# Kernel optimization log

Measured on AMD Instinct MI355X. Metric: run time of the kernel, lower is better.

Reference implementation:

```python
import jax, jax.numpy as jnp
from jax import lax
import numpy as np

L = 2          # num_delimiter_layers
H = 8          # num q/kv heads
MIN_CL = 3
MAX_CL = 16

def rms_norm(x, w, eps=1e-6):
    return x * lax.rsqrt(jnp.mean(x * x, axis=-1, keepdims=True) + eps) * w

def rope(t):
    # t: [B, H, S, Dh], GPT-NeoX style half-split rotation, theta=10000
    Dh, S = t.shape[-1], t.shape[-2]
    half = Dh // 2
    inv = 1.0 / (10000.0 ** (jnp.arange(half, dtype=jnp.float32) / half))
    fr = jnp.arange(S, dtype=jnp.float32)[:, None] * inv  # [S, half]
    cos, sin = jnp.cos(fr), jnp.sin(fr)
    t1, t2 = t[..., :half], t[..., half:]
    return jnp.concatenate([t1 * cos - t2 * sin, t1 * sin + t2 * cos], axis=-1)

def chunk_ids_one(flags):
    # flags: [S] bool (probs > 0.5). Returns per-position chunk id and num chunks.
    S = flags.shape[0]
    # ends take value p+1 for flagged p; fallback to a single end at S-1 if none.
    has_end = jnp.zeros(S + 1, bool).at[1:].set(flags)
    fallback = jnp.zeros(S + 1, bool).at[S - 1].set(True)
    has_end = jnp.where(flags.any(), has_end, fallback)
    idx = jnp.where(has_end, jnp.arange(S + 1), S + 1)  # S+1 = sentinel > any cap
    nxt = lax.associative_scan(jnp.minimum, idx, reverse=True)  # nxt[e] = min end >= e
    def step(carry, t):
        cur_end, cid = carry
        def new(_):
            cap = jnp.minimum(t + MAX_CL, S)
            e = nxt[t + 1]                       # smallest end > t
            e = jnp.where(e <= cap, e, cap)
            e = jnp.where(e - t < MIN_CL, jnp.minimum(t + MIN_CL, S), e)
            return e, cid + 1
        new_end, new_cid = lax.cond(t == cur_end, new, lambda _: (cur_end, cid), None)
        return (new_end, new_cid), new_cid
    (_, last), ids = lax.scan(step, (jnp.int32(0), jnp.int32(-1)), jnp.arange(S, dtype=jnp.int32))
    return ids, last + 1

def _forward(x, ln1, Wq, Wk, Wv, Wo, ln2, W1, W2, head_w, head_b):
    B, S, D = x.shape
    Dh = D // H
    causal = jnp.tril(jnp.ones((S, S), bool))
    scale = 1.0 / np.sqrt(Dh)
    for l in range(L):
        h = rms_norm(x, ln1[l])
        def split_heads(t):
            return t.reshape(B, S, H, Dh).transpose(0, 2, 1, 3)
        q = rope(split_heads(h @ Wq[l]))
        k = rope(split_heads(h @ Wk[l]))
        v = split_heads(h @ Wv[l])
        scores = jnp.einsum('bhqd,bhkd->bhqk', q, k) * scale
        scores = jnp.where(causal, scores, jnp.finfo(scores.dtype).min)
        attn = jax.nn.softmax(scores, axis=-1)
        o = jnp.einsum('bhqk,bhkd->bhqd', attn, v)
        o = o.transpose(0, 2, 1, 3).reshape(B, S, D)
        x = x + o @ Wo[l]
        h = rms_norm(x, ln2[l])
        x = x + jax.nn.gelu(h @ W1[l], approximate=False) @ W2[l]
    logits = (x @ head_w).squeeze(-1) + head_b[0]
    probs = jax.nn.sigmoid(logits)
    chunk_len_loss = jnp.mean(jnp.sum(probs, axis=1))
    return x, probs, chunk_len_loss

def setup_inputs():
    key = jax.random.key(0)
    ks = jax.random.split(key, 10)
    B, S, D = 4, 2048, 512
    F = 4 * D
    sc = 0.02
    return {
        'x': jax.random.normal(ks[0], (B, S, D), jnp.float32),
        'x_ids': jax.random.randint(ks[1], (B, S), 0, 256),
        'ln1': jnp.ones((L, D), jnp.float32),
        'Wq': jax.random.normal(ks[2], (L, D, D), jnp.float32) * sc,
        'Wk': jax.random.normal(ks[3], (L, D, D), jnp.float32) * sc,
        'Wv': jax.random.normal(ks[4], (L, D, D), jnp.float32) * sc,
        'Wo': jax.random.normal(ks[5], (L, D, D), jnp.float32) * sc,
        'ln2': jnp.ones((L, D), jnp.float32),
        'W1': jax.random.normal(ks[6], (L, D, F), jnp.float32) * sc,
        'W2': jax.random.normal(ks[7], (L, F, D), jnp.float32) * sc,
        'head_w': jax.random.normal(ks[8], (D, 1), jnp.float32) * sc,
        'head_b': jnp.zeros((1,), jnp.float32),
    }

def reference(x, x_ids, ln1, Wq, Wk, Wv, Wo, ln2, W1, W2, head_w, head_b):
    B, S, D = x.shape
    x_t, probs, chunk_len_loss = _forward(x, ln1, Wq, Wk, Wv, Wo, ln2, W1, W2, head_w, head_b)
    flags = probs > 0.5
    ids, n_chunks = jax.vmap(chunk_ids_one)(flags)  # ids: [B,S] int32
    # chunks partition [0,S), so block-diagonal mask == chunk-id equality
    attention_masks = ids[:, :, None] == ids[:, None, :]
    # per-batch mean chunk length = S / num_chunks (lengths sum to S)
    avg_chunk_len = jnp.mean(jnp.float32(S) / n_chunks.astype(jnp.float32))
    return (x_t, x_ids, avg_chunk_len, attention_masks, chunk_len_loss)
```

## Files before the change

### kernel.cpp

```cpp
#include <hip/hip_runtime.h>
#include <math.h>

#define S_LEN 2048
#define DMODEL 512
#define NHEAD 8
#define DH 64
#define FDIM 2048

typedef unsigned short ushort_t;
typedef __attribute__((ext_vector_type(8))) short short8_t;
typedef __attribute__((ext_vector_type(4))) float float4_t;

#define MFMA16(a, b, c) __builtin_amdgcn_mfma_f32_16x16x32_bf16(a, b, c, 0, 0, 0)



__device__ __forceinline__ ushort_t f2bf(float x) {
    unsigned u = __float_as_uint(x);
    return (ushort_t)((u + 0x7fffu + ((u >> 16) & 1u)) >> 16);
}
__device__ __forceinline__ float bf2f(ushort_t h) {
    return __uint_as_float((unsigned)h << 16);
}
__device__ __forceinline__ float gelu_f(float x) {
    return 0.5f * x * (1.0f + erff(x * 0.70710678118654752440f));
}
__device__ __forceinline__ void gl_lds16(const void* g, void* l) {
    __builtin_amdgcn_global_load_lds(
        (const __attribute__((address_space(1))) void*)g,
        (__attribute__((address_space(3))) void*)l, 16, 0, 0);
}

template<int CTRL>
__device__ __forceinline__ float dpp_mov(float x) {
    return __int_as_float(__builtin_amdgcn_mov_dpp(__float_as_int(x), CTRL, 0xF, 0xF, true));
}
__device__ __forceinline__ float dpp_max16(float x) {
    x = fmaxf(x, dpp_mov<0xB1>(x));
    x = fmaxf(x, dpp_mov<0x4E>(x));
    x = fmaxf(x, dpp_mov<0x141>(x));
    x = fmaxf(x, dpp_mov<0x140>(x));
    return x;
}
__device__ __forceinline__ float dpp_sum16(float x) {
    x += dpp_mov<0xB1>(x);
    x += dpp_mov<0x4E>(x);
    x += dpp_mov<0x141>(x);
    x += dpp_mov<0x140>(x);
    return x;
}

__device__ __forceinline__ void stage_tile(const ushort_t* __restrict__ g, int rs,
                                           ushort_t* __restrict__ s, int w, int lane) {
    #pragma unroll
    for (int j = 0; j < 2; ++j) {
        const int c = (w * 2 + j) * 64 + lane;
        const int kk = c >> 8, row = (c >> 2) & 63, q = c & 3;
        const int qs = q ^ ((row >> 1) & 3);
        gl_lds16(g + (size_t)row * rs + kk * 32 + qs * 8, s + c * 8);
    }
}

__global__ __launch_bounds__(256) void copy_init_k(const int* __restrict__ x_ids,
                                                   float* __restrict__ out) {
    const int i = blockIdx.x * 256 + threadIdx.x;
    const int4 id4 = ((const int4*)x_ids)[i];
    ((float4*)out)[1048576 + i] =
        make_float4((float)id4.x, (float)id4.y, (float)id4.z, (float)id4.w);
    if (i == 0) { out[4202496] = 0.0f; out[20979713] = 0.0f; }
}

__global__ __launch_bounds__(256) void rope_tab_k(float2* __restrict__ tab) {
    const int i = blockIdx.x * 256 + threadIdx.x;
    const int s = i >> 5, f = i & 31;
    float inv = powf(10000.0f, -(float)f * (1.0f / 32.0f));
    float sn, cs;
    sincosf((float)s * inv, &sn, &cs);
    tab[i] = make_float2(cs, sn);
}

__global__ __launch_bounds__(256) void tsplit_all_k(const float* __restrict__ Wq,
                                                    const float* __restrict__ Wk,
                                                    const float* __restrict__ Wv,
                                                    const float* __restrict__ Wo,
                                                    const float* __restrict__ W1,
                                                    const float* __restrict__ W2,
                                                    ushort_t* __restrict__ wbuf) {
    __shared__ float T[32][33];
    const int bid = blockIdx.x;
    const int l = bid / 3072;
    const int r = bid % 3072;
    ushort_t* lb = wbuf + (size_t)l * 6291456;
    const float* W; ushort_t* Thi; ushort_t* Tlo; int K, N, ntn, rr;
    if (r < 768) {
        const int which = r >> 8; rr = r & 255;
        W = (which == 0 ? Wq : which == 1 ? Wk : Wv) + (size_t)l * 262144;
        Thi = lb + which * 262144; Tlo = lb + 786432 + which * 262144;
        K = 512; N = 512; ntn = 16;
    } else if (r < 1024) {
        rr = r - 768; W = Wo + (size_t)l * 262144;
        Thi = lb + 1572864; Tlo = lb + 1835008; K = 512; N = 512; ntn = 16;
    } else if (r < 2048) {
        rr = r - 1024; W = W1 + (size_t)l * 1048576;
        Thi = lb + 2097152; Tlo = lb + 3145728; K = 512; N = 2048; ntn = 64;
    } else {
        rr = r - 2048; W = W2 + (size_t)l * 1048576;
        Thi = lb + 4194304; Tlo = lb + 5242880; K = 2048; N = 512; ntn = 16;
    }
    const int n0 = (rr % ntn) * 32, k0 = (rr / ntn) * 32;
    const int tx = threadIdx.x & 31, ty = threadIdx.x >> 5;
    #pragma unroll
    for (int i = 0; i < 4; ++i)
        T[ty + 8 * i][tx] = W[(size_t)(k0 + ty + 8 * i) * N + n0 + tx];
    __syncthreads();
    #pragma unroll
    for (int i = 0; i < 4; ++i) {
        const int n = ty + 8 * i;
        float x = T[tx][n];
        ushort_t hi = f2bf(x);
        Thi[(size_t)(n0 + n) * K + k0 + tx] = hi;
        Tlo[(size_t)(n0 + n) * K + k0 + tx] = f2bf(x - bf2f(hi));
    }
}

__global__ __launch_bounds__(256) void rmsnorm_split_k(const float* __restrict__ x,
                                                       const float* __restrict__ w,
                                                       ushort_t* __restrict__ hhi,
                                                       ushort_t* __restrict__ hlo) {
    __shared__ float red[4];
    const int tid = threadIdx.x;
    const int b = blockIdx.x;
    const size_t row = (size_t)((b & 7) * 1024 + (b >> 3));
    const float* xr = x + row * DMODEL;
    float2 v = *(const float2*)(xr + tid * 2);
    float ss = v.x * v.x + v.y * v.y;
    #pragma unroll
    for (int off = 32; off; off >>= 1) ss += __shfl_down(ss, off);
    if ((tid & 63) == 0) red[tid >> 6] = ss;
    __syncthreads();
    float tot = red[0] + red[1] + red[2] + red[3];
    float rs = 1.0f / sqrtf(tot * (1.0f / 512.0f) + 1e-6f);
    float2 wv = *(const float2*)(w + tid * 2);
    float y0 = v.x * rs * wv.x, y1 = v.y * rs * wv.y;
    ushort_t h0 = f2bf(y0), h1 = f2bf(y1);
    ushort_t l0 = f2bf(y0 - bf2f(h0)), l1 = f2bf(y1 - bf2f(h1));
    *(unsigned*)(hhi + row * DMODEL + tid * 2) = ((unsigned)h1 << 16) | h0;
    *(unsigned*)(hlo + row * DMODEL + tid * 2) = ((unsigned)l1 << 16) | l0;
}

template<int EPI, int TN>
__global__ __launch_bounds__(256) void gemm_s(const ushort_t* __restrict__ Ahi,
                                              const ushort_t* __restrict__ Alo,
                                              const ushort_t* __restrict__ Bhi,
                                              const ushort_t* __restrict__ Blo,
                                              int K, int N,
                                              float* __restrict__ C,
                                              const float* __restrict__ Cin,
                                              ushort_t* __restrict__ Chi,
                                              ushort_t* __restrict__ Clo,
                                              ushort_t* __restrict__ oqh,
                                              ushort_t* __restrict__ oql,
                                              ushort_t* __restrict__ okh,
                                              ushort_t* __restrict__ okl,
                                              ushort_t* __restrict__ ovh,
                                              const float2* __restrict__ rtab) {
    constexpr int MT = (TN == 128) ? 4 : 2;
    constexpr int NBUF = (TN == 64) ? 3 : 2;
    constexpr int LPS = (TN == 64) ? 6 : 8;
    __shared__ __align__(16) ushort_t sAhi[NBUF][4096], sAlo[NBUF][4096];
    __shared__ __align__(16) ushort_t sBhi[NBUF][TN * 32], sBlo[NBUF][TN * 32];
    const int tid = threadIdx.x;
    const int lane = tid & 63, w = tid >> 6;
    const int wm = (TN == 128) ? (w >> 1) : w;
    const int wn = (TN == 128) ? (w & 1) : 0;
    const int nbn = N / TN;
    const int id = blockIdx.x;
    const int jj = id >> 3;
    const int bm = (id & 7) * 8 + jj / nbn;
    const int bn = jj % nbn;
    const int sm = lane >> 2;
    const int sk = ((lane & 3) ^ ((sm >> 1) & 3)) * 8;
    const int fr = lane & 15;
    const int fq = lane >> 4;
    const int fko = (fq ^ ((fr >> 1) & 3)) * 8;

    auto stage = [&](int buf, int kt) {
        #pragma unroll
        for (int j = 0; j < 2; ++j) {
            const int chunk = w * 2 + j;
            const int mr = chunk * 16 + sm;
            const size_t ga = (size_t)(bm * 128 + mr) * K + kt + sk;
            gl_lds16(Ahi + ga, &sAhi[buf][chunk * 512]);
            gl_lds16(Alo + ga, &sAlo[buf][chunk * 512]);
        }
        #pragma unroll
        for (int j = 0; j < TN / 64; ++j) {
            const int chunk = w * (TN / 64) + j;
            const int mr = chunk * 16 + sm;
            const size_t gb = (size_t)(bn * TN + mr) * K + kt + sk;
            gl_lds16(Bhi + gb, &sBhi[buf][chunk * 512]);
            gl_lds16(Blo + gb, &sBlo[buf][chunk * 512]);
        }
    };

    float4_t acc[MT][4] = {};

    if (NBUF == 3) {
        stage(0, 0);
        if (32 < K) stage(1, 32);
    } else {
        stage(0, 0);
    }
    int cur = 0;
    for (int kt = 0; kt < K; kt += 32) {
        if (NBUF == 2) {
            __syncthreads();
            if (kt + 32 < K) stage(cur ^ 1, kt + 32);
        } else {
            if (kt + 32 < K)
                asm volatile("s_waitcnt vmcnt(%0) lgkmcnt(0)" :: "i"(LPS) : "memory");
            else
                asm volatile("s_waitcnt vmcnt(0) lgkmcnt(0)" ::: "memory");
            __builtin_amdgcn_s_barrier();
            if (kt + 64 < K) stage((cur + 2) % 3, kt + 64);
        }
        short8_t ah[MT], al[MT], bh[4], bl[4];
        #pragma unroll
        for (int t = 0; t < MT; ++t) {
            const int ao = (wm * (MT * 16) + t * 16 + fr) * 32 + fko;
            ah[t] = *(const short8_t*)&sAhi[cur][ao];
            al[t] = *(const short8_t*)&sAlo[cur][ao];
        }
        #pragma unroll
        for (int t = 0; t < 4; ++t) {
            const int bo = (wn * 64 + t * 16 + fr) * 32 + fko;
            bh[t] = *(const short8_t*)&sBhi[cur][bo];
            bl[t] = *(const short8_t*)&sBlo[cur][bo];
        }
        #pragma unroll
        for (int tm = 0; tm < MT; ++tm)
            #pragma unroll
            for (int tn = 0; tn < 4; ++tn) {
                acc[tm][tn] = MFMA16(ah[tm], bh[tn], acc[tm][tn]);
                acc[tm][tn] = MFMA16(al[tm], bh[tn], acc[tm][tn]);
                acc[tm][tn] = MFMA16(ah[tm], bl[tn], acc[tm][tn]);
            }
        cur = (cur + 1) % NBUF;
    }

    if (EPI == 0) {
        const int cb = bn * 128 + wn * 64;
        const int mat = cb >> 9;
        const int hh = (cb >> 6) & 7;
        #pragma unroll
        for (int tm = 0; tm < MT; ++tm) {
            #pragma unroll
            for (int r = 0; r < 4; ++r) {
                const int mg = bm * 128 + wm * (MT * 16) + tm * 16 + fq * 4 + r;
                const int b = mg >> 11, s = mg & 2047;
                const int bhh = b * NHEAD + hh;
                if (mat < 2) {
                    ushort_t* dhi = (mat == 0) ? oqh : okh;
                    ushort_t* dlo = (mat == 0) ? oql : okl;
                    const size_t base = ((size_t)bhh * S_LEN + s) * DH;
                    #pragma unroll
                    for (int tn = 0; tn < 2; ++tn) {
                        const int d1 = tn * 16 + fr;
                        const float v1 = acc[tm][tn][r], v2 = acc[tm][tn + 2][r];
                        const float2 t = rtab[s * 32 + d1];
                        float r1 = v1 * t.x - v2 * t.y;
                        float r2 = v1 * t.y + v2 * t.x;
                        if (mat == 0) { r1 *= 0.125f; r2 *= 0.125f; }
                        ushort_t h1 = f2bf(r1), h2 = f2bf(r2);
                        dhi[base + d1]      = h1;
                        dlo[base + d1]      = f2bf(r1 - bf2f(h1));
                        dhi[base + d1 + 32] = h2;
                        dlo[base + d1 + 32] = f2bf(r2 - bf2f(h2));
                    }
                } else {
                    #pragma unroll
                    for (int tn = 0; tn < 4; ++tn) {
                        const int d = tn * 16 + fr;
                        const size_t off = ((size_t)bhh * DH + d) * S_LEN + s;
                        ovh[off] = f2bf(acc[tm][tn][r]);
                    }
                }
            }
        }
    } else {
        #pragma unroll
        for (int tm = 0; tm < MT; ++tm) {
            #pragma unroll
            for (int tn = 0; tn < 4; ++tn) {
                const int cb = bn * TN + wn * 64 + tn * 16;
                #pragma unroll
                for (int r = 0; r < 4; ++r) {
                    const int mg = bm * 128 + wm * (MT * 16) + tm * 16 + fq * 4 + r;
                    const float val = acc[tm][tn][r];
                    const size_t off = (size_t)mg * N + cb + fr;
                    if (EPI == 1) {
                        C[off] = Cin[off] + val;
                    } else {
                        const float g = gelu_f(val);
                        const ushort_t hi = f2bf(g);
                        Chi[off] = hi;
                        Clo[off] = f2bf(g - bf2f(hi));
                    }
                }
            }
        }
    }
}

__global__ __launch_bounds__(256) void attn_k(const ushort_t* __restrict__ qhi,
                                              const ushort_t* __restrict__ qlo,
                                              const ushort_t* __restrict__ khi,
                                              const ushort_t* __restrict__ klo,
                                              const ushort_t* __restrict__ vthi,
                                              ushort_t* __restrict__ Ohi,
                                              ushort_t* __restrict__ Olo) {
    __shared__ __align__(16) ushort_t sKh[2][4096], sKl[2][4096];
    __shared__ __align__(16) ushort_t sVh[2][4096], sPh[4096];
    const int tid = threadIdx.x, lane = tid & 63, w = tid >> 6;
    const int fr = lane & 15, fq = lane >> 4;
    const int fko = (fq ^ ((fr >> 1) & 3)) * 8;
    const int bidx = blockIdx.x;
    const int bh = bidx & 31;
    const int p = bidx >> 5;

    auto stage3 = [&](int buf, int kt) {
        const size_t ko = ((size_t)bh * S_LEN + kt * 64) * DH;
        stage_tile(khi + ko, 64, sKh[buf], w, lane);
        stage_tile(klo + ko, 64, sKl[buf], w, lane);
        const size_t vo = (size_t)bh * DH * S_LEN + kt * 64;
        stage_tile(vthi + vo, S_LEN, sVh[buf], w, lane);
    };

    for (int half = 0; half < 2; ++half) {
        const int qt = half ? p : 31 - p;

        short8_t qfh[2], qfl[2];
        {
            const size_t base = ((size_t)bh * S_LEN + qt * 64 + w * 16 + fr) * DH + fq * 8;
            qfh[0] = *(const short8_t*)(qhi + base);
            qfh[1] = *(const short8_t*)(qhi + base + 32);
            qfl[0] = *(const short8_t*)(qlo + base);
            qfl[1] = *(const short8_t*)(qlo + base + 32);
        }

        float m_r[4], l_r[4];
        float4_t oacc[4] = {};
        #pragma unroll
        for (int r = 0; r < 4; ++r) { m_r[r] = -INFINITY; l_r[r] = 0.0f; }

        __syncthreads();
        stage3(0, 0);
        int cur = 0;

        for (int kt = 0; kt <= qt; ++kt) {
            const bool diag = (kt == qt);
            __syncthreads();
            if (kt < qt) stage3(cur ^ 1, kt + 1);

            float4_t sacc[4] = {};
            __builtin_amdgcn_s_setprio(1);
            #pragma unroll
            for (int kk = 0; kk < 2; ++kk) {
                #pragma unroll
                for (int n = 0; n < 4; ++n) {
                    const int bb = kk * 2048 + (n * 16 + fr) * 32 + fko;
                    short8_t kh2 = *(const short8_t*)&sKh[cur][bb];
                    short8_t kl2 = *(const short8_t*)&sKl[cur][bb];
                    sacc[n] = MFMA16(qfh[kk], kh2, sacc[n]);
                    sacc[n] = MFMA16(qfl[kk], kh2, sacc[n]);
                    sacc[n] = MFMA16(qfh[kk], kl2, sacc[n]);
                }
            }
            __builtin_amdgcn_s_setprio(0);

            #pragma unroll
            for (int r = 0; r < 4; ++r) {
                const int rowl = fq * 4 + r;
                const int qrow = w * 16 + rowl;
                const int psw = (qrow >> 1) & 3;
                float sv[4], mx = -INFINITY;
                #pragma unroll
                for (int n = 0; n < 4; ++n) {
                    sv[n] = sacc[n][r];
                    if (diag && (n * 16 + fr) > qrow) sv[n] = -1e30f;
                    mx = fmaxf(mx, sv[n]);
                }
                mx = dpp_max16(mx);
                const float mn = fmaxf(m_r[r], mx);
                const float alp = __expf(m_r[r] - mn);
                m_r[r] = mn;
                float ls = 0.0f;
                #pragma unroll
                for (int n = 0; n < 4; ++n) {
                    const float pv = __expf(sv[n] - mn);
                    const int c0 = (n & 1) * 16 + fr;
                    const int idx = (n >> 1) * 2048 + qrow * 32 + ((c0 >> 3) ^ psw) * 8 + (c0 & 7);
                    sPh[idx] = f2bf(pv);
                    ls += pv;
                }
                ls = dpp_sum16(ls);
                l_r[r] = alp * l_r[r] + ls;
                #pragma unroll
                for (int n = 0; n < 4; ++n) oacc[n][r] *= alp;
            }

            __builtin_amdgcn_s_setprio(1);
            #pragma unroll
            for (int kkj = 0; kkj < 2; ++kkj) {
                short8_t ph = *(const short8_t*)&sPh[kkj * 2048 + (w * 16 + fr) * 32 + fko];
                #pragma unroll
                for (int n = 0; n < 4; ++n) {
                    short8_t vh = *(const short8_t*)&sVh[cur][kkj * 2048 + (n * 16 + fr) * 32 + fko];
                    oacc[n] = MFMA16(ph, vh, oacc[n]);
                }
            }
            __builtin_amdgcn_s_setprio(0);
            cur ^= 1;
        }

        const int b = bh >> 3, hh = bh & 7;
        #pragma unroll
        for (int r = 0; r < 4; ++r) {
            const float inv_l = 1.0f / l_r[r];
            const int s = qt * 64 + w * 16 + fq * 4 + r;
            const size_t base = ((size_t)b * S_LEN + s) * DMODEL + hh * DH;
            #pragma unroll
            for (int n = 0; n < 4; ++n) {
                const float y = oacc[n][r] * inv_l;
                const ushort_t h = f2bf(y);
                Ohi[base + n * 16 + fr] = h;
                Olo[base + n * 16 + fr] = f2bf(y - bf2f(h));
            }
        }
    }
}

__global__ __launch_bounds__(256) void head_k(const float* __restrict__ x,
                                              const float* __restrict__ w,
                                              const float* __restrict__ b,
                                              float* __restrict__ probs) {
    const int tid = threadIdx.x;
    const int lane = tid & 63;
    const size_t row = (size_t)blockIdx.x * 4 + (tid >> 6);
    const float* xr = x + row * DMODEL;
    float acc = 0.0f;
    #pragma unroll
    for (int i = 0; i < 8; ++i) acc += xr[lane + i * 64] * w[lane + i * 64];
    #pragma unroll
    for (int off = 32; off; off >>= 1) acc += __shfl_down(acc, off);
    if (lane == 0)
        probs[row] = 1.0f / (1.0f + expf(-(acc + b[0])));
}

__global__ __launch_bounds__(256) void chunk_k(const float* __restrict__ probs,
                                               int* __restrict__ ids,
                                               float* __restrict__ avg_out,
                                               float* __restrict__ loss_out) {
    __shared__ ushort_t nxA[2052], nxB[2052];
    __shared__ ushort_t lift[10][2052];
    __shared__ float lred[4];
    __shared__ int anyf;
    const int b = blockIdx.x, tid = threadIdx.x;
    const float* pr = probs + (size_t)b * S_LEN;
    if (tid == 0) anyf = 0;
    __syncthreads();
    int loc = 0;
    float lsum = 0.0f;
    for (int t = tid; t < S_LEN; t += 256) {
        const float p = pr[t];
        loc |= (p > 0.5f) ? 1 : 0;
        lsum += p;
    }
    if (loc) atomicOr(&anyf, 1);
    #pragma unroll
    for (int off = 32; off; off >>= 1) lsum += __shfl_down(lsum, off);
    if ((tid & 63) == 0) lred[tid >> 6] = lsum;
    __syncthreads();
    if (tid == 0)
        atomicAdd(loss_out, (lred[0] + lred[1] + lred[2] + lred[3]) * 0.25f);
    const int any = anyf;
    for (int i = tid; i <= S_LEN; i += 256) {
        const bool he = any ? (i >= 1 && pr[i - 1] > 0.5f) : (i == S_LEN - 1);
        nxA[i] = he ? (ushort_t)i : (ushort_t)(S_LEN + 1);
    }
    __syncthreads();
    ushort_t* src = nxA;
    ushort_t* dst = nxB;
    for (int d = 1; d <= 2048; d <<= 1) {
        for (int i = tid; i <= S_LEN; i += 256) {
            ushort_t v = src[i];
            if (i + d <= S_LEN) { ushort_t u2 = src[i + d]; v = u2 < v ? u2 : v; }
            dst[i] = v;
        }
        __syncthreads();
        ushort_t* tmp = src; src = dst; dst = tmp;
    }
    for (int t = tid; t < S_LEN; t += 256) {
        int cap = t + 16; if (cap > S_LEN) cap = S_LEN;
        int e = src[t + 1];
        if (e > cap) e = cap;
        if (e - t < 3) { e = t + 3; if (e > S_LEN) e = S_LEN; }
        lift[0][t] = (ushort_t)e;
    }
    if (tid == 0) lift[0][S_LEN] = (ushort_t)S_LEN;
    __syncthreads();
    for (int j = 1; j < 10; ++j) {
        for (int t = tid; t <= S_LEN; t += 256)
            lift[j][t] = lift[j - 1][lift[j - 1][t]];
        __syncthreads();
    }
    for (int t = tid; t < S_LEN; t += 256) {
        int pos = 0, cid = 0;
        #pragma unroll
        for (int j = 9; j >= 0; --j) {
            const int p2 = lift[j][pos];
            if (p2 <= t) { pos = p2; cid += (1 << j); }
        }
        ids[(size_t)b * S_LEN + t] = cid;
        if (t == S_LEN - 1) atomicAdd(avg_out, 512.0f / (float)(cid + 1));
    }
}

__global__ __launch_bounds__(256) void masks_k(const int* __restrict__ ids,
                                               float* __restrict__ mask) {
    const int bq = blockIdx.x;
    const int b = bq >> 11;
    const int myid = ids[bq];
    const int* idr = ids + (size_t)b * S_LEN;
    float* mr = mask + (size_t)bq * S_LEN;
    for (int k = threadIdx.x; k < S_LEN; k += 256)
        mr[k] = (idr[k] == myid) ? 1.0f : 0.0f;
}

extern "C" void kernel_launch(void* const* d_in, const int* in_sizes, int n_in,
                              void* d_out, int out_size, void* d_ws, size_t ws_size,
                              hipStream_t stream) {
    (void)in_sizes; (void)n_in; (void)out_size; (void)ws_size;
    const float* x      = (const float*)d_in[0];
    const int*   x_ids  = (const int*)d_in[1];
    const float* ln1    = (const float*)d_in[2];
    const float* Wq     = (const float*)d_in[3];
    const float* Wk     = (const float*)d_in[4];
    const float* Wv     = (const float*)d_in[5];
    const float* Wo     = (const float*)d_in[6];
    const float* ln2    = (const float*)d_in[7];
    const float* W1     = (const float*)d_in[8];
    const float* W2     = (const float*)d_in[9];
    const float* head_w = (const float*)d_in[10];
    const float* head_b = (const float*)d_in[11];

    float* out = (float*)d_out;
    ushort_t* u = (ushort_t*)d_ws;
    ushort_t* qh   = u;
    ushort_t* ql   = u + 4194304;
    ushort_t* kh   = u + 8388608;
    ushort_t* kl   = u + 12582912;
    ushort_t* vth  = u + 16777216;
    ushort_t* ohi  = u + 25165824;
    ushort_t* olo  = u + 29360128;
    ushort_t* hhi  = u + 33554432;
    ushort_t* hlo  = u + 37748736;
    ushort_t* ffhi = u;
    ushort_t* fflo = u + 16777216;
    float*    probs = (float*)(u + 41943040);
    int*      ids   = (int*)(u + 41943040 + 16384);
    ushort_t* wbuf     = (ushort_t*)(out + 4202512);
    float2*   rope_tab = (float2*)(wbuf + 12582912);
    float* xbuf = out;

    copy_init_k<<<8, 256, 0, stream>>>(x_ids, out);
    rope_tab_k<<<256, 256, 0, stream>>>(rope_tab);
    tsplit_all_k<<<6144, 256, 0, stream>>>(Wq, Wk, Wv, Wo, W1, W2, wbuf);

    for (int l = 0; l < 2; ++l) {
        ushort_t* lb = wbuf + (size_t)l * 6291456;
        ushort_t* qkvT_hi = lb;
        ushort_t* qkvT_lo = lb + 786432;
        ushort_t* woT_hi  = lb + 1572864;
        ushort_t* woT_lo  = lb + 1835008;
        ushort_t* w1T_hi  = lb + 2097152;
        ushort_t* w1T_lo  = lb + 3145728;
        ushort_t* w2T_hi  = lb + 4194304;
        ushort_t* w2T_lo  = lb + 5242880;
        const float* xin = (l == 0) ? x : xbuf;

        rmsnorm_split_k<<<8192, 256, 0, stream>>>(xin, ln1 + l * DMODEL, hhi, hlo);
        gemm_s<0, 128><<<768, 256, 0, stream>>>(hhi, hlo, qkvT_hi, qkvT_lo, 512, 1536,
                                                nullptr, nullptr, nullptr, nullptr,
                                                qh, ql, kh, kl, vth, rope_tab);
        attn_k<<<512, 256, 0, stream>>>(qh, ql, kh, kl, vth, ohi, olo);
        gemm_s<1, 64><<<512, 256, 0, stream>>>(ohi, olo, woT_hi, woT_lo, 512, 512,
                                               xbuf, xin, nullptr, nullptr,
                                               nullptr, nullptr, nullptr, nullptr, nullptr, nullptr);
        rmsnorm_split_k<<<8192, 256, 0, stream>>>(xbuf, ln2 + l * DMODEL, hhi, hlo);
        gemm_s<2, 128><<<1024, 256, 0, stream>>>(hhi, hlo, w1T_hi, w1T_lo, 512, 2048,
                                                 nullptr, nullptr, ffhi, fflo,
                                                 nullptr, nullptr, nullptr, nullptr, nullptr, nullptr);
        gemm_s<1, 64><<<512, 256, 0, stream>>>(ffhi, fflo, w2T_hi, w2T_lo, 2048, 512,
                                               xbuf, xbuf, nullptr, nullptr,
                                               nullptr, nullptr, nullptr, nullptr, nullptr, nullptr);
    }

    head_k<<<2048, 256, 0, stream>>>(xbuf, head_w, head_b, probs);
    chunk_k<<<4, 256, 0, stream>>>(probs, ids, out + 4202496, out + 20979713);
    masks_k<<<8192, 256, 0, stream>>>(ids, out + 4202497);
}
```

Before: 781.5 us.

## Launch one attention block per query tile and single-buffer K-low in LDS

Measured after the change: 774.3 us. No clear change (-0.9%).

```diff
diff --git a/kernel.cpp b/kernel.cpp
--- a/kernel.cpp
+++ b/kernel.cpp
@@ -319,123 +319,122 @@
                                               const ushort_t* __restrict__ vthi,
                                               ushort_t* __restrict__ Ohi,
                                               ushort_t* __restrict__ Olo) {
-    __shared__ __align__(16) ushort_t sKh[2][4096], sKl[2][4096];
-    __shared__ __align__(16) ushort_t sVh[2][4096], sPh[4096];
+    __shared__ __align__(16) ushort_t sKh[2][4096], sVh[2][4096];
+    __shared__ __align__(16) ushort_t sKl[4096], sPh[4096];
     const int tid = threadIdx.x, lane = tid & 63, w = tid >> 6;
     const int fr = lane & 15, fq = lane >> 4;
     const int fko = (fq ^ ((fr >> 1) & 3)) * 8;
     const int bidx = blockIdx.x;
     const int bh = bidx & 31;
-    const int p = bidx >> 5;
-
-    auto stage3 = [&](int buf, int kt) {
-        const size_t ko = ((size_t)bh * S_LEN + kt * 64) * DH;
-        stage_tile(khi + ko, 64, sKh[buf], w, lane);
-        stage_tile(klo + ko, 64, sKl[buf], w, lane);
-        const size_t vo = (size_t)bh * DH * S_LEN + kt * 64;
-        stage_tile(vthi + vo, S_LEN, sVh[buf], w, lane);
-    };
-
-    for (int half = 0; half < 2; ++half) {
-        const int qt = half ? p : 31 - p;
-
-        short8_t qfh[2], qfl[2];
-        {
-            const size_t base = ((size_t)bh * S_LEN + qt * 64 + w * 16 + fr) * DH + fq * 8;
-            qfh[0] = *(const short8_t*)(qhi + base);
-            qfh[1] = *(const short8_t*)(qhi + base + 32);
-            qfl[0] = *(const short8_t*)(qlo + base);
-            qfl[1] = *(const short8_t*)(qlo + base + 32);
-        }
-
-        float m_r[4], l_r[4];
-        float4_t oacc[4] = {};
-        #pragma unroll
-        for (int r = 0; r < 4; ++r) { m_r[r] = -INFINITY; l_r[r] = 0.0f; }
-
+    const int qt = 31 - (bidx >> 5);
+
+    short8_t qfh[2], qfl[2];
+    {
+        const size_t base = ((size_t)bh * S_LEN + qt * 64 + w * 16 + fr) * DH + fq * 8;
+        qfh[0] = *(const short8_t*)(qhi + base);
+        qfh[1] = *(const short8_t*)(qhi + base + 32);
+        qfl[0] = *(const short8_t*)(qlo + base);
+        qfl[1] = *(const short8_t*)(qlo + base + 32);
+    }
+
+    float m_r[4], l_r[4];
+    float4_t oacc[4] = {};
+    #pragma unroll
+    for (int r = 0; r < 4; ++r) { m_r[r] = -INFINITY; l_r[r] = 0.0f; }
+
+    stage_tile(khi + (size_t)bh * S_LEN * DH, 64, sKh[0], w, lane);
+    stage_tile(klo + (size_t)bh * S_LEN * DH, 64, sKl, w, lane);
+    stage_tile(vthi + (size_t)bh * DH * S_LEN, S_LEN, sVh[0], w, lane);
+    int cur = 0;
+
+    for (int kt = 0; kt <= qt; ++kt) {
+        const bool diag = (kt == qt);
         __syncthreads();
-        stage3(0, 0);
-        int cur = 0;
-
-        for (int kt = 0; kt <= qt; ++kt) {
-            const bool diag = (kt == qt);
+        if (kt < qt) {
+            const size_t ko = ((size_t)bh * S_LEN + (kt + 1) * 64) * DH;
+            stage_tile(khi + ko, 64, sKh[cur ^ 1], w, lane);
+            const size_t vo = (size_t)bh * DH * S_LEN + (kt + 1) * 64;
+            stage_tile(vthi + vo, S_LEN, sVh[cur ^ 1], w, lane);
+        }
+
+        float4_t sacc[4] = {};
+        __builtin_amdgcn_s_setprio(1);
+        #pragma unroll
+        for (int kk = 0; kk < 2; ++kk) {
+            #pragma unroll
+            for (int n = 0; n < 4; ++n) {
+                const int bb = kk * 2048 + (n * 16 + fr) * 32 + fko;
+                short8_t kh2 = *(const short8_t*)&sKh[cur][bb];
+                short8_t kl2 = *(const short8_t*)&sKl[bb];
+                sacc[n] = MFMA16(qfh[kk], kh2, sacc[n]);
+                sacc[n] = MFMA16(qfl[kk], kh2, sacc[n]);
+                sacc[n] = MFMA16(qfh[kk], kl2, sacc[n]);
+            }
+        }
+        __builtin_amdgcn_s_setprio(0);
+
+        #pragma unroll
+        for (int r = 0; r < 4; ++r) {
+            const int qrow = w * 16 + fq * 4 + r;
+            const int psw = (qrow >> 1) & 3;
+            float sv[4], mx = -INFINITY;
+            #pragma unroll
+            for (int n = 0; n < 4; ++n) {
+                sv[n] = sacc[n][r];
+                if (diag && (n * 16 + fr) > qrow) sv[n] = -1e30f;
+                mx = fmaxf(mx, sv[n]);
+            }
+            mx = dpp_max16(mx);
+            const float mn = fmaxf(m_r[r], mx);
+            const float alp = __expf(m_r[r] - mn);
+            m_r[r] = mn;
+            float ls = 0.0f;
+            #pragma unroll
+            for (int n = 0; n < 4; ++n) {
+                const float pv = __expf(sv[n] - mn);
+                const int c0 = (n & 1) * 16 + fr;
+                const int idx = (n >> 1) * 2048 + qrow * 32 + ((c0 >> 3) ^ psw) * 8 + (c0 & 7);
+                sPh[idx] = f2bf(pv);
+                ls += pv;
+            }
+            ls = dpp_sum16(ls);
+            l_r[r] = alp * l_r[r] + ls;
+            #pragma unroll
+            for (int n = 0; n < 4; ++n) oacc[n][r] *= alp;
+        }
+
+        if (kt < qt) {
             __syncthreads();
-            if (kt < qt) stage3(cur ^ 1, kt + 1);
-
-            float4_t sacc[4] = {};
-            __builtin_amdgcn_s_setprio(1);
-            #pragma unroll
-            for (int kk = 0; kk < 2; ++kk) {
-                #pragma unroll
-                for (int n = 0; n < 4; ++n) {
-                    const int bb = kk * 2048 + (n * 16 + fr) * 32 + fko;
-                    short8_t kh2 = *(const short8_t*)&sKh[cur][bb];
-                    short8_t kl2 = *(const short8_t*)&sKl[cur][bb];
-                    sacc[n] = MFMA16(qfh[kk], kh2, sacc[n]);
-                    sacc[n] = MFMA16(qfl[kk], kh2, sacc[n]);
-                    sacc[n] = MFMA16(qfh[kk], kl2, sacc[n]);
-                }
+            const size_t ko = ((size_t)bh * S_LEN + (kt + 1) * 64) * DH;
+            stage_tile(klo + ko, 64, sKl, w, lane);
+        }
+
+        __builtin_amdgcn_s_setprio(1);
+        #pragma unroll
+        for (int kkj = 0; kkj < 2; ++kkj) {
+            short8_t ph = *(const short8_t*)&sPh[kkj * 2048 + (w * 16 + fr) * 32 + fko];
+            #pragma unroll
+            for (int n = 0; n < 4; ++n) {
+                short8_t vh = *(const short8_t*)&sVh[cur][kkj * 2048 + (n * 16 + fr) * 32 + fko];
+                oacc[n] = MFMA16(ph, vh, oacc[n]);
             }
-            __builtin_amdgcn_s_setprio(0);
-
-            #pragma unroll
-            for (int r = 0; r < 4; ++r) {
-                const int rowl = fq * 4 + r;
-                const int qrow = w * 16 + rowl;
-                const int psw = (qrow >> 1) & 3;
-                float sv[4], mx = -INFINITY;
-                #pragma unroll
-                for (int n = 0; n < 4; ++n) {
-                    sv[n] = sacc[n][r];
-                    if (diag && (n * 16 + fr) > qrow) sv[n] = -1e30f;
-                    mx = fmaxf(mx, sv[n]);
-                }
-                mx = dpp_max16(mx);
-                const float mn = fmaxf(m_r[r], mx);
-                const float alp = __expf(m_r[r] - mn);
-                m_r[r] = mn;
-                float ls = 0.0f;
-                #pragma unroll
-                for (int n = 0; n < 4; ++n) {
-                    const float pv = __expf(sv[n] - mn);
-                    const int c0 = (n & 1) * 16 + fr;
-                    const int idx = (n >> 1) * 2048 + qrow * 32 + ((c0 >> 3) ^ psw) * 8 + (c0 & 7);
-                    sPh[idx] = f2bf(pv);
-                    ls += pv;
-                }
-                ls = dpp_sum16(ls);
-                l_r[r] = alp * l_r[r] + ls;
-                #pragma unroll
-                for (int n = 0; n < 4; ++n) oacc[n][r] *= alp;
-            }
-
-            __builtin_amdgcn_s_setprio(1);
-            #pragma unroll
-            for (int kkj = 0; kkj < 2; ++kkj) {
-                short8_t ph = *(const short8_t*)&sPh[kkj * 2048 + (w * 16 + fr) * 32 + fko];
-                #pragma unroll
-                for (int n = 0; n < 4; ++n) {
-                    short8_t vh = *(const short8_t*)&sVh[cur][kkj * 2048 + (n * 16 + fr) * 32 + fko];
-                    oacc[n] = MFMA16(ph, vh, oacc[n]);
-                }
-            }
-            __builtin_amdgcn_s_setprio(0);
-            cur ^= 1;
-        }
-
-        const int b = bh >> 3, hh = bh & 7;
-        #pragma unroll
-        for (int r = 0; r < 4; ++r) {
-            const float inv_l = 1.0f / l_r[r];
-            const int s = qt * 64 + w * 16 + fq * 4 + r;
-            const size_t base = ((size_t)b * S_LEN + s) * DMODEL + hh * DH;
-            #pragma unroll
-            for (int n = 0; n < 4; ++n) {
-                const float y = oacc[n][r] * inv_l;
-                const ushort_t h = f2bf(y);
-                Ohi[base + n * 16 + fr] = h;
-                Olo[base + n * 16 + fr] = f2bf(y - bf2f(h));
-            }
+        }
+        __builtin_amdgcn_s_setprio(0);
+        cur ^= 1;
+    }
+
+    const int b = bh >> 3, hh = bh & 7;
+    #pragma unroll
+    for (int r = 0; r < 4; ++r) {
+        const float inv_l = 1.0f / l_r[r];
+        const int s = qt * 64 + w * 16 + fq * 4 + r;
+        const size_t base = ((size_t)b * S_LEN + s) * DMODEL + hh * DH;
+        #pragma unroll
+        for (int n = 0; n < 4; ++n) {
+            const float y = oacc[n][r] * inv_l;
+            const ushort_t h = f2bf(y);
+            Ohi[base + n * 16 + fr] = h;
+            Olo[base + n * 16 + fr] = f2bf(y - bf2f(h));
         }
     }
 }
@@ -593,7 +592,7 @@
         gemm_s<0, 128><<<768, 256, 0, stream>>>(hhi, hlo, qkvT_hi, qkvT_lo, 512, 1536,
                                                 nullptr, nullptr, nullptr, nullptr,
                                                 qh, ql, kh, kl, vth, rope_tab);
-        attn_k<<<512, 256, 0, stream>>>(qh, ql, kh, kl, vth, ohi, olo);
+        attn_k<<<1024, 256, 0, stream>>>(qh, ql, kh, kl, vth, ohi, olo);
         gemm_s<1, 64><<<512, 256, 0, stream>>>(ohi, olo, woT_hi, woT_lo, 512, 512,
                                                xbuf, xin, nullptr, nullptr,
                                                nullptr, nullptr, nullptr, nullptr, nullptr, nullptr);
```
